# Kernel tuning notes

Measured on AMD Instinct MI355X. Metric: run time of the kernel, lower is better.

The kernel has to match this reference:

```python
import jax, jax.numpy as jnp
import numpy as np

L, H, C, D, B, OUT = 3, 4, 128, 128, 64, 128  # layers, heads, out_ch per head, in_dim, graphs, out_dim
NEG_SLOPE = 0.2
EPS = 1e-5


def _layernorm(x, g, b):
    mu = x.mean(-1, keepdims=True)
    var = ((x - mu) ** 2).mean(-1, keepdims=True)
    return (x - mu) * jax.lax.rsqrt(var + EPS) * g + b


def setup_inputs() -> dict:
    key = jax.random.key(0)
    ks = jax.random.split(key, 20)
    N, E = 50000, 400000
    x = jax.random.normal(ks[0], (N, D), jnp.float32)
    edge_index = jax.random.randint(ks[1], (2, E), 0, N, jnp.int64)
    batch = jnp.sort(jax.random.randint(ks[2], (N,), 0, B, jnp.int64))
    s = 1.0 / np.sqrt(D)
    inp = dict(x=x, edge_index=edge_index, batch=batch)
    inp["Wl"] = jax.random.normal(ks[3], (L, H, C, D), jnp.float32) * s
    inp["bl"] = jnp.zeros((L, H, C), jnp.float32)
    inp["Wr"] = jax.random.normal(ks[4], (L, H, C, D), jnp.float32) * s
    inp["br"] = jnp.zeros((L, H, C), jnp.float32)
    inp["att"] = jax.random.normal(ks[5], (L, H, C), jnp.float32) * (1.0 / np.sqrt(C))
    inp["conv_bias"] = jnp.zeros((L, C), jnp.float32)
    inp["ln_gamma"] = jnp.ones((L, C), jnp.float32)
    inp["ln_beta"] = jnp.zeros((L, C), jnp.float32)
    inp["W1"] = jax.random.normal(ks[6], (2 * C, C), jnp.float32) * (1.0 / np.sqrt(C))
    inp["b1"] = jnp.zeros((2 * C,), jnp.float32)
    inp["W2"] = jax.random.normal(ks[7], (OUT, 2 * C), jnp.float32) * (1.0 / np.sqrt(2 * C))
    inp["b2"] = jnp.zeros((OUT,), jnp.float32)
    inp["og"] = jnp.ones((OUT,), jnp.float32)
    inp["ob"] = jnp.zeros((OUT,), jnp.float32)
    return inp


def reference(x, edge_index, batch, Wl, bl, Wr, br, att, conv_bias, ln_gamma, ln_beta, W1, b1, W2, b2, og, ob):
    N = x.shape[0]
    loops = jnp.arange(N, dtype=edge_index.dtype)
    src = jnp.concatenate([edge_index[0], loops])  # [E+N]
    dst = jnp.concatenate([edge_index[1], loops])
    h = x  # input_proj is Identity (node_feat_dim == hidden_dim)
    for l in range(L):
        xl = jnp.einsum('nd,hcd->nhc', h, Wl[l]) + bl[l]  # [N,H,C]
        xr = jnp.einsum('nd,hcd->nhc', h, Wr[l]) + br[l]
        e = jax.nn.leaky_relu(xl[src] + xr[dst], NEG_SLOPE)  # [E+N,H,C]
        logits = jnp.einsum('ehc,hc->eh', e, att[l])  # [E+N,H]
        m = jax.ops.segment_max(logits, dst, num_segments=N)  # [N,H]
        p = jnp.exp(logits - m[dst])
        denom = jax.ops.segment_sum(p, dst, num_segments=N)
        alpha = p / denom[dst]  # segment softmax (self loops guarantee denom>0)
        out = jax.ops.segment_sum(xl[src] * alpha[:, :, None], dst, num_segments=N)  # [N,H,C]
        out = out.mean(axis=1) + conv_bias[l]  # concat=False -> mean over heads
        out = jax.nn.relu(_layernorm(out, ln_gamma[l], ln_beta[l]))
        h = h + out  # residual
    # global mean pool
    sums = jax.ops.segment_sum(h, batch, num_segments=B)
    cnt = jax.ops.segment_sum(jnp.ones((N,), h.dtype), batch, num_segments=B)
    g = sums / jnp.maximum(cnt, 1.0)[:, None]
    # MLP head + out norm
    g = jax.nn.gelu(g @ W1.T + b1, approximate=False) @ W2.T + b2
    return _layernorm(g, og, ob)
```

## Files before the change

### kernel.cpp

```cpp
#include <hip/hip_runtime.h>
#include <hip/hip_bf16.h>

typedef __bf16 bf16x8 __attribute__((ext_vector_type(8)));
typedef float f32x4 __attribute__((ext_vector_type(4)));
typedef float f32x2 __attribute__((ext_vector_type(2)));

#define EPS 1e-5f

static __device__ __forceinline__ int lower_bound_i(const int* __restrict__ arr, int n, int val) {
  int lo = 0, hi = n;
  while (lo < hi) { int mid = (lo + hi) >> 1; if (arr[mid] < val) lo = mid + 1; else hi = mid; }
  return lo;
}

__global__ void detect_dtypes(const unsigned* __restrict__ xw, const unsigned* __restrict__ eiw,
                              int* __restrict__ flags) {
  __shared__ int s_bf16, s_i64nz;
  int t = threadIdx.x;
  if (t == 0) { s_bf16 = 0; s_i64nz = 0; }
  __syncthreads();
  unsigned w = xw[t * 97];
  unsigned lo = w & 0xFFFFu;
  unsigned e = (lo >> 7) & 0xFF;
  int looks_bf16 = (lo == 0u) || (e >= 0x6A && e <= 0x86);
  atomicAdd(&s_bf16, looks_bf16);
  int k = t * 1031;
  int nz = (eiw[2 * k + 1] != 0u) ? 1 : 0;
  atomicAdd(&s_i64nz, nz);
  __syncthreads();
  if (t == 0) {
    flags[0] = (s_bf16 >= 192) ? 1 : 0;
    flags[1] = (s_i64nz == 0) ? 1 : 0;
  }
}

__global__ void canon_x(const void* __restrict__ src, float* __restrict__ h_f32,
                        __bf16* __restrict__ h_bf, int n, const int* __restrict__ flags) {
  int i = blockIdx.x * blockDim.x + threadIdx.x;
  if (i >= n) return;
  float v;
  if (flags[0]) v = (float)((const __bf16*)src)[i];
  else          v = ((const float*)src)[i];
  h_f32[i] = v;
  h_bf[i] = (__bf16)v;
}

struct ParamDesc { const void* src[12]; int off[13]; };

__global__ void canon_params(ParamDesc pd, float* __restrict__ dst, const int* __restrict__ flags,
                             int total) {
  int i = blockIdx.x * blockDim.x + threadIdx.x;
  if (i >= total) return;
  int s = 0;
#pragma unroll
  for (int k = 1; k < 12; k++) if (i >= pd.off[k]) s = k;
  int j = i - pd.off[s];
  const void* sp = pd.src[s];
  dst[i] = flags[0] ? (float)((const __bf16*)sp)[j] : ((const float*)sp)[j];
}

__global__ void canon_bf16(const void* __restrict__ src, __bf16* __restrict__ dst, int n,
                           const int* __restrict__ flags) {
  int i = blockIdx.x * blockDim.x + threadIdx.x;
  if (i >= n) return;
  if (flags[0]) dst[i] = ((const __bf16*)src)[i];
  else          dst[i] = (__bf16)((const float*)src)[i];
}

__global__ void canon_i32(const void* __restrict__ src, int* __restrict__ dst, int n,
                          const int* __restrict__ flags) {
  int i = blockIdx.x * blockDim.x + threadIdx.x;
  if (i >= n) return;
  if (flags[1]) dst[i] = (int)((const long long*)src)[i];
  else          dst[i] = ((const int*)src)[i];
}

__global__ void count_deg(const int* __restrict__ ei, int E, int N, int* __restrict__ deg) {
  int e = blockIdx.x * blockDim.x + threadIdx.x;
  if (e >= E + N) return;
  int d = (e < E) ? ei[E + e] : (e - E);
  atomicAdd(&deg[d], 1);
}

__global__ __launch_bounds__(256) void block_sums(const int* __restrict__ deg,
                                                  int* __restrict__ bsum, int N) {
  __shared__ int sh[256];
  int i = blockIdx.x * 256 + threadIdx.x;
  int t = threadIdx.x;
  sh[t] = (i < N) ? deg[i] : 0;
  __syncthreads();
  for (int off = 128; off > 0; off >>= 1) {
    if (t < off) sh[t] += sh[t + off];
    __syncthreads();
  }
  if (t == 0) bsum[blockIdx.x] = sh[0];
}

__global__ __launch_bounds__(256) void scan_bsums(const int* __restrict__ bsum,
                                                  int* __restrict__ bpref, int nblocks,
                                                  int* __restrict__ offs, int N) {
  __shared__ int sh[256];
  int t = threadIdx.x;
  int carry = 0;
  for (int base = 0; base < nblocks; base += 256) {
    int idx = base + t;
    int v = (idx < nblocks) ? bsum[idx] : 0;
    sh[t] = v;
    __syncthreads();
    for (int off = 1; off < 256; off <<= 1) {
      int u = (t >= off) ? sh[t - off] : 0;
      __syncthreads();
      sh[t] += u;
      __syncthreads();
    }
    if (idx < nblocks) bpref[idx] = carry + sh[t] - v;
    carry += sh[255];
    __syncthreads();
  }
  if (t == 0) offs[N] = carry;
}

__global__ __launch_bounds__(256) void write_offs(const int* __restrict__ deg,
                                                  const int* __restrict__ bpref,
                                                  int* __restrict__ offs,
                                                  int* __restrict__ cursor, int N) {
  __shared__ int sh[256];
  int i = blockIdx.x * 256 + threadIdx.x;
  int t = threadIdx.x;
  int v = (i < N) ? deg[i] : 0;
  sh[t] = v;
  __syncthreads();
  for (int off = 1; off < 256; off <<= 1) {
    int u = (t >= off) ? sh[t - off] : 0;
    __syncthreads();
    sh[t] += u;
    __syncthreads();
  }
  if (i < N) {
    int ex = bpref[blockIdx.x] + sh[t] - v;
    offs[i] = ex;
    cursor[i] = ex;
  }
}

__global__ void fill_csr(const int* __restrict__ ei, int E, int N,
                         int* __restrict__ cursor, int* __restrict__ csr_src) {
  int e = blockIdx.x * blockDim.x + threadIdx.x;
  if (e >= E + N) return;
  int s, d;
  if (e < E) { s = ei[e]; d = ei[E + e]; } else { s = e - E; d = e - E; }
  int pos = atomicAdd(&cursor[d], 1);
  csr_src[pos] = s;
}

__global__ __launch_bounds__(256) void gemm_xlr(
    const __bf16* __restrict__ A, const __bf16* __restrict__ Wl,
    const __bf16* __restrict__ Wr, const float* __restrict__ bl,
    const float* __restrict__ br, __bf16* __restrict__ out, int Nrows) {
  __shared__ __bf16 As[128][72];
  __shared__ __bf16 Bs[128][72];
  const int jb = blockIdx.y;
  const __bf16* Wbase = (jb < 4) ? (Wl + (size_t)jb * 128 * 128) : (Wr + (size_t)(jb - 4) * 128 * 128);
  const float* biasbase = (jb < 4) ? (bl + jb * 128) : (br + (jb - 4) * 128);
  const int row0 = blockIdx.x * 128;
  const int tid = threadIdx.x;
  const int lane = tid & 63, wave = tid >> 6;
  const int wm = wave >> 1, wn = wave & 1;

  f32x4 zero4 = {0.f, 0.f, 0.f, 0.f};
  f32x4 acc[4][4];
#pragma unroll
  for (int mi = 0; mi < 4; mi++)
#pragma unroll
    for (int ni = 0; ni < 4; ni++) acc[mi][ni] = zero4;

  for (int kc = 0; kc < 2; kc++) {
    __syncthreads();
#pragma unroll
    for (int p = 0; p < 4; p++) {
      int r = (tid >> 3) + p * 32;
      int cg = (tid & 7) * 8;
      int gr = row0 + r;
      bf16x8 av;
      if (gr < Nrows) av = *(const bf16x8*)(A + (size_t)gr * 128 + kc * 64 + cg);
      else {
#pragma unroll
        for (int j = 0; j < 8; j++) av[j] = (__bf16)0.0f;
      }
      *(bf16x8*)(&As[r][cg]) = av;
      bf16x8 bv = *(const bf16x8*)(Wbase + (size_t)r * 128 + kc * 64 + cg);
      *(bf16x8*)(&Bs[r][cg]) = bv;
    }
    __syncthreads();
#pragma unroll
    for (int s = 0; s < 2; s++) {
      bf16x8 af[4], bfr[4];
      int kofs = s * 32 + ((lane >> 4) * 8);
#pragma unroll
      for (int i = 0; i < 4; i++) {
        af[i]  = *(const bf16x8*)(&As[wm * 64 + i * 16 + (lane & 15)][kofs]);
        bfr[i] = *(const bf16x8*)(&Bs[wn * 64 + i * 16 + (lane & 15)][kofs]);
      }
#pragma unroll
      for (int mi = 0; mi < 4; mi++)
#pragma unroll
        for (int ni = 0; ni < 4; ni++)
          acc[mi][ni] = __builtin_amdgcn_mfma_f32_16x16x32_bf16(af[mi], bfr[ni], acc[mi][ni], 0, 0, 0);
    }
  }
#pragma unroll
  for (int mi = 0; mi < 4; mi++) {
#pragma unroll
    for (int ni = 0; ni < 4; ni++) {
      int col_l = wn * 64 + ni * 16 + (lane & 15);
      int gj = jb * 128 + col_l;
      float bias = biasbase[col_l];
#pragma unroll
      for (int r = 0; r < 4; r++) {
        int row_l = wm * 64 + mi * 16 + (lane >> 4) * 4 + r;
        int gr = row0 + row_l;
        if (gr < Nrows) out[(size_t)gr * 1024 + gj] = (__bf16)(acc[mi][ni][r] + bias);
      }
    }
  }
}

__global__ __launch_bounds__(256) void gat_fused(
    const __bf16* __restrict__ comb, const float* __restrict__ att,
    const int* __restrict__ offs, const int* __restrict__ csr_src,
    const float* __restrict__ conv_bias, const float* __restrict__ gamma,
    const float* __restrict__ beta, float* __restrict__ h_f32,
    __bf16* __restrict__ h_bf, int N) {
  int wid = blockIdx.x * 4 + (threadIdx.x >> 6);
  int lane = threadIdx.x & 63;
  if (wid >= N) return;
  int n = wid;
  f32x2 xr2[4], at2[4];
  bf16x8 xrv = *(const bf16x8*)(comb + (size_t)n * 1024 + 512 + lane * 8);
  float4 a0 = *(const float4*)(att + lane * 8);
  float4 a1 = *(const float4*)(att + lane * 8 + 4);
  at2[0] = f32x2{a0.x, a0.y}; at2[1] = f32x2{a0.z, a0.w};
  at2[2] = f32x2{a1.x, a1.y}; at2[3] = f32x2{a1.z, a1.w};
#pragma unroll
  for (int j = 0; j < 4; j++) xr2[j] = f32x2{(float)xrv[2 * j], (float)xrv[2 * j + 1]};

  int off0 = offs[n], off1 = offs[n + 1];
  float m = -1e30f, l = 0.f;
  f32x2 acc2[4];
#pragma unroll
  for (int j = 0; j < 4; j++) acc2[j] = f32x2{0.f, 0.f};

  const __bf16* cb_base = comb;

  auto process = [&](const bf16x8& xv) {
    f32x2 x2[4];
    f32x2 t2 = f32x2{0.f, 0.f};
#pragma unroll
    for (int j = 0; j < 4; j++) {
      x2[j] = f32x2{(float)xv[2 * j], (float)xv[2 * j + 1]};
      f32x2 z = x2[j] + xr2[j];
      f32x2 lz = __builtin_elementwise_max(z, 0.2f * z);
      t2 = t2 + lz * at2[j];
    }
    float t = t2[0] + t2[1];
    t += __shfl_xor(t, 1);
    t += __shfl_xor(t, 2);
    t += __shfl_xor(t, 4);
    t += __shfl_xor(t, 8);
    float mn = fmaxf(m, t);
    float c = __expf(m - mn);
    float p = __expf(t - mn);
    l = fmaf(l, c, p);
    f32x2 c2 = f32x2{c, c}, p2 = f32x2{p, p};
#pragma unroll
    for (int j = 0; j < 4; j++) acc2[j] = acc2[j] * c2 + p2 * x2[j];
    m = mn;
  };

  int pos = off0;
  for (; pos + 2 <= off1; pos += 2) {
    int s0 = csr_src[pos], s1 = csr_src[pos + 1];
    bf16x8 xa = *(const bf16x8*)(cb_base + (size_t)s0 * 1024 + lane * 8);
    bf16x8 xb = *(const bf16x8*)(cb_base + (size_t)s1 * 1024 + lane * 8);
    process(xa);
    process(xb);
  }
  if (pos < off1) {
    int s0 = csr_src[pos];
    bf16x8 xa = *(const bf16x8*)(cb_base + (size_t)s0 * 1024 + lane * 8);
    process(xa);
  }

  float invl = 1.0f / fmaxf(l, 1e-30f);
  float acc[8];
#pragma unroll
  for (int j = 0; j < 4; j++) {
    acc[2 * j]     = acc2[j][0] * invl;
    acc[2 * j + 1] = acc2[j][1] * invl;
  }
#pragma unroll
  for (int j = 0; j < 8; j++) {
    acc[j] += __shfl_xor(acc[j], 16);
    acc[j] += __shfl_xor(acc[j], 32);
  }
  int c0 = (lane & 15) * 8;
  float v[8];
  float s = 0.f, s2 = 0.f;
#pragma unroll
  for (int j = 0; j < 8; j++) {
    v[j] = acc[j] * 0.25f + conv_bias[c0 + j];
    s += v[j]; s2 += v[j] * v[j];
  }
  s  += __shfl_xor(s, 1);  s2 += __shfl_xor(s2, 1);
  s  += __shfl_xor(s, 2);  s2 += __shfl_xor(s2, 2);
  s  += __shfl_xor(s, 4);  s2 += __shfl_xor(s2, 4);
  s  += __shfl_xor(s, 8);  s2 += __shfl_xor(s2, 8);
  float mu = s * (1.f / 128.f);
  float var = fmaxf(s2 * (1.f / 128.f) - mu * mu, 0.f);
  float rs = rsqrtf(var + EPS);
  if (lane < 16) {
    float4 o0, o1;
    bf16x8 hb;
    float hn[8];
#pragma unroll
    for (int j = 0; j < 8; j++) {
      float o = (v[j] - mu) * rs * gamma[c0 + j] + beta[c0 + j];
      o = o > 0.f ? o : 0.f;
      hn[j] = h_f32[(size_t)n * 128 + c0 + j] + o;
      hb[j] = (__bf16)hn[j];
    }
    o0.x = hn[0]; o0.y = hn[1]; o0.z = hn[2]; o0.w = hn[3];
    o1.x = hn[4]; o1.y = hn[5]; o1.z = hn[6]; o1.w = hn[7];
    *(float4*)(h_f32 + (size_t)n * 128 + c0) = o0;
    *(float4*)(h_f32 + (size_t)n * 128 + c0 + 4) = o1;
    *(bf16x8*)(h_bf + (size_t)n * 128 + c0) = hb;
  }
}

__global__ __launch_bounds__(128) void pool(const float* __restrict__ h_f32,
                                            const int* __restrict__ batch, int N,
                                            float* __restrict__ g_sum) {
  int g = blockIdx.x >> 3, slice = blockIdx.x & 7;
  int c = threadIdx.x;
  int r0 = lower_bound_i(batch, N, g);
  int r1 = lower_bound_i(batch, N, g + 1);
  int len = r1 - r0;
  if (len <= 0) return;
  int per = (len + 7) / 8;
  int s0 = r0 + slice * per;
  int s1 = min(s0 + per, r1);
  if (s0 >= s1) return;
  float acc = 0.f;
  for (int r = s0; r < s1; r++) acc += h_f32[(size_t)r * 128 + c];
  atomicAdd(&g_sum[g * 128 + c], acc);
}

__global__ __launch_bounds__(256) void mlp_head(
    const float* __restrict__ g_sum, const int* __restrict__ batch, int N,
    const float* __restrict__ W1, const float* __restrict__ b1,
    const float* __restrict__ W2, const float* __restrict__ b2,
    const float* __restrict__ og, const float* __restrict__ ob,
    void* __restrict__ outv, const int* __restrict__ flags) {
  __shared__ float gld[128];
  __shared__ float hid[256];
  __shared__ float olds[128];
  __shared__ float red[2];
  int b = blockIdx.x, t = threadIdx.x;
  int r0 = lower_bound_i(batch, N, b);
  int r1 = lower_bound_i(batch, N, b + 1);
  int len = r1 - r0;
  float cntf = (float)(len < 1 ? 1 : len);
  if (t < 128) gld[t] = g_sum[b * 128 + t] / cntf;
  __syncthreads();
  float sacc = b1[t];
  for (int d = 0; d < 128; d++) sacc = fmaf(gld[d], W1[(size_t)t * 128 + d], sacc);
  hid[t] = 0.5f * sacc * (1.f + erff(sacc * 0.70710678118654752f));
  __syncthreads();
  if (t < 128) {
    float o = b2[t];
    for (int k = 0; k < 256; k++) o = fmaf(hid[k], W2[(size_t)t * 256 + k], o);
    olds[t] = o;
  }
  __syncthreads();
  if (t < 64) {
    float a = olds[t], bb = olds[t + 64];
    float s = a + bb, s2 = a * a + bb * bb;
    for (int off = 32; off; off >>= 1) { s += __shfl_down(s, off); s2 += __shfl_down(s2, off); }
    if (t == 0) { red[0] = s * (1.f / 128.f); red[1] = s2 * (1.f / 128.f); }
  }
  __syncthreads();
  if (t < 128) {
    float mu = red[0];
    float var = fmaxf(red[1] - mu * mu, 0.f);
    float rs = rsqrtf(var + EPS);
    float o = (olds[t] - mu) * rs * og[t] + ob[t];
    if (flags[0]) ((__bf16*)outv)[b * 128 + t] = (__bf16)o;
    else          ((float*)outv)[b * 128 + t] = o;
  }
}

extern "C" void kernel_launch(void* const* d_in, const int* in_sizes, int n_in,
                              void* d_out, int out_size, void* d_ws, size_t ws_size,
                              hipStream_t stream) {
  const int D = 128, B = 64;
  const int N = in_sizes[0] / D;
  const int E = in_sizes[1] / 2;
  const int EN = E + N;
  const int nsb = (N + 255) / 256;

  char* p = (char*)d_ws;
  auto alloc = [&](size_t bytes) {
    char* r = p; p += (bytes + 255) & ~(size_t)255; return (void*)r;
  };
  int* flags     = (int*)alloc(256);
  float* h_f32   = (float*)alloc((size_t)N * 128 * 4);
  __bf16* h_bf   = (__bf16*)alloc((size_t)N * 128 * 2);
  __bf16* comb   = (__bf16*)alloc((size_t)N * 1024 * 2);
  int* deg       = (int*)alloc((size_t)N * 4);
  int* offs      = (int*)alloc((size_t)(N + 1) * 4);
  int* cursor    = (int*)alloc((size_t)N * 4);
  int* csr_src   = (int*)alloc((size_t)EN * 4);
  float* g_sum   = (float*)alloc((size_t)B * 128 * 4);
  int* ei32      = (int*)alloc((size_t)2 * E * 4);
  int* bat32     = (int*)alloc((size_t)N * 4);
  int* bsum      = (int*)alloc((size_t)nsb * 4);
  int* bpref     = (int*)alloc((size_t)nsb * 4);
  __bf16* w_bf   = (__bf16*)alloc((size_t)2 * 196608 * 2);
  float* params  = (float*)alloc((size_t)71936 * 4);

  float* bl_c  = params + 0;
  float* br_c  = params + 1536;
  float* att_c = params + 3072;
  float* cb_c  = params + 4608;
  float* g_c   = params + 4992;
  float* b_c   = params + 5376;
  float* W1_c  = params + 5760;
  float* b1_c  = params + 38528;
  float* W2_c  = params + 38784;
  float* b2_c  = params + 71552;
  float* og_c  = params + 71680;
  float* ob_c  = params + 71808;

  detect_dtypes<<<1, 256, 0, stream>>>((const unsigned*)d_in[0], (const unsigned*)d_in[1], flags);

  canon_x<<<(N * 128 + 255) / 256, 256, 0, stream>>>(d_in[0], h_f32, h_bf, N * 128, flags);

  ParamDesc pd;
  const int srcidx[12] = {4, 6, 7, 8, 9, 10, 11, 12, 13, 14, 15, 16};
  const int sizes12[12] = {1536, 1536, 1536, 384, 384, 384, 32768, 256, 32768, 128, 128, 128};
  int cum = 0;
  for (int k = 0; k < 12; k++) { pd.src[k] = d_in[srcidx[k]]; pd.off[k] = cum; cum += sizes12[k]; }
  pd.off[12] = cum;
  canon_params<<<(cum + 255) / 256, 256, 0, stream>>>(pd, params, flags, cum);

  canon_bf16<<<(196608 + 255) / 256, 256, 0, stream>>>(d_in[3], w_bf, 196608, flags);
  canon_bf16<<<(196608 + 255) / 256, 256, 0, stream>>>(d_in[5], w_bf + 196608, 196608, flags);

  canon_i32<<<(2 * E + 255) / 256, 256, 0, stream>>>(d_in[1], ei32, 2 * E, flags);
  canon_i32<<<(N + 255) / 256, 256, 0, stream>>>(d_in[2], bat32, N, flags);

  hipMemsetAsync(deg, 0, (size_t)N * 4, stream);
  hipMemsetAsync(g_sum, 0, (size_t)B * 128 * 4, stream);

  count_deg<<<(EN + 255) / 256, 256, 0, stream>>>(ei32, E, N, deg);
  block_sums<<<nsb, 256, 0, stream>>>(deg, bsum, N);
  scan_bsums<<<1, 256, 0, stream>>>(bsum, bpref, nsb, offs, N);
  write_offs<<<nsb, 256, 0, stream>>>(deg, bpref, offs, cursor, N);
  fill_csr<<<(EN + 255) / 256, 256, 0, stream>>>(ei32, E, N, cursor, csr_src);

  for (int l = 0; l < 3; l++) {
    gemm_xlr<<<dim3((N + 127) / 128, 8), 256, 0, stream>>>(
        h_bf, w_bf + (size_t)l * 65536, w_bf + 196608 + (size_t)l * 65536,
        bl_c + l * 512, br_c + l * 512, comb, N);
    gat_fused<<<(N + 3) / 4, 256, 0, stream>>>(comb, att_c + l * 512, offs, csr_src,
        cb_c + l * 128, g_c + l * 128, b_c + l * 128, h_f32, h_bf, N);
  }
  pool<<<B * 8, 128, 0, stream>>>(h_f32, bat32, N, g_sum);
  mlp_head<<<B, 256, 0, stream>>>(g_sum, bat32, N, W1_c, b1_c, W2_c, b2_c, og_c, ob_c, d_out, flags);
}
```

Baseline: 646.7 us.

## Drop online-softmax max tracking, use DPP row reductions, fuse int canonicalization

The GAT aggregation kernel replaces its online softmax rescaling with a clamped direct exponential, removing the running max and per-edge rescale of accumulators. Cross-lane sums switch from shuffles to DPP row operations, and the edge loop issues four gathers at a time. Integer input conversion and degree counting merge into one kernel. The clamp changes numerics if logits exceed the clamp range.

```diff
diff --git a/kernel.cpp b/kernel.cpp
--- a/kernel.cpp
+++ b/kernel.cpp
@@ -11,6 +11,19 @@
   int lo = 0, hi = n;
   while (lo < hi) { int mid = (lo + hi) >> 1; if (arr[mid] < val) lo = mid + 1; else hi = mid; }
   return lo;
+}
+
+template <int CTRL>
+static __device__ __forceinline__ float dpp_add(float x) {
+  int s = __builtin_amdgcn_mov_dpp(__float_as_int(x), CTRL, 0xF, 0xF, true);
+  return x + __int_as_float(s);
+}
+static __device__ __forceinline__ float row16_reduce(float t) {
+  t = dpp_add<0xB1>(t);
+  t = dpp_add<0x4E>(t);
+  t = dpp_add<0x141>(t);
+  t = dpp_add<0x140>(t);
+  return t;
 }
 
 __global__ void detect_dtypes(const unsigned* __restrict__ xw, const unsigned* __restrict__ eiw,
@@ -67,19 +80,23 @@
   else          dst[i] = (__bf16)((const float*)src)[i];
 }
 
-__global__ void canon_i32(const void* __restrict__ src, int* __restrict__ dst, int n,
-                          const int* __restrict__ flags) {
+__global__ void canon_ints(const void* __restrict__ ei_src, const void* __restrict__ bat_src,
+                           int* __restrict__ ei32, int* __restrict__ bat32,
+                           int* __restrict__ deg, int E, int N, const int* __restrict__ flags) {
   int i = blockIdx.x * blockDim.x + threadIdx.x;
-  if (i >= n) return;
-  if (flags[1]) dst[i] = (int)((const long long*)src)[i];
-  else          dst[i] = ((const int*)src)[i];
-}
-
-__global__ void count_deg(const int* __restrict__ ei, int E, int N, int* __restrict__ deg) {
-  int e = blockIdx.x * blockDim.x + threadIdx.x;
-  if (e >= E + N) return;
-  int d = (e < E) ? ei[E + e] : (e - E);
-  atomicAdd(&deg[d], 1);
+  int total = 2 * E + N;
+  if (i >= total) return;
+  int i64 = flags[1];
+  if (i < 2 * E) {
+    int v = i64 ? (int)((const long long*)ei_src)[i] : ((const int*)ei_src)[i];
+    ei32[i] = v;
+    if (i >= E) atomicAdd(&deg[v], 1);
+  } else {
+    int j = i - 2 * E;
+    int v = i64 ? (int)((const long long*)bat_src)[j] : ((const int*)bat_src)[j];
+    bat32[j] = v;
+    atomicAdd(&deg[j], 1);
+  }
 }
 
 __global__ __launch_bounds__(256) void block_sums(const int* __restrict__ deg,
@@ -245,12 +262,12 @@
   for (int j = 0; j < 4; j++) xr2[j] = f32x2{(float)xrv[2 * j], (float)xrv[2 * j + 1]};
 
   int off0 = offs[n], off1 = offs[n + 1];
-  float m = -1e30f, l = 0.f;
+  float l = 0.f;
   f32x2 acc2[4];
 #pragma unroll
   for (int j = 0; j < 4; j++) acc2[j] = f32x2{0.f, 0.f};
 
-  const __bf16* cb_base = comb;
+  const __bf16* lane_base = comb + lane * 8;
 
   auto process = [&](const bf16x8& xv) {
     f32x2 x2[4];
@@ -263,31 +280,28 @@
       t2 = t2 + lz * at2[j];
     }
     float t = t2[0] + t2[1];
-    t += __shfl_xor(t, 1);
-    t += __shfl_xor(t, 2);
-    t += __shfl_xor(t, 4);
-    t += __shfl_xor(t, 8);
-    float mn = fmaxf(m, t);
-    float c = __expf(m - mn);
-    float p = __expf(t - mn);
-    l = fmaf(l, c, p);
-    f32x2 c2 = f32x2{c, c}, p2 = f32x2{p, p};
-#pragma unroll
-    for (int j = 0; j < 4; j++) acc2[j] = acc2[j] * c2 + p2 * x2[j];
-    m = mn;
+    t = row16_reduce(t);
+    t = fminf(fmaxf(t, -60.f), 60.f);
+    float p = __expf(t);
+    l += p;
+    f32x2 p2 = f32x2{p, p};
+#pragma unroll
+    for (int j = 0; j < 4; j++) acc2[j] = acc2[j] + p2 * x2[j];
   };
 
   int pos = off0;
-  for (; pos + 2 <= off1; pos += 2) {
+  for (; pos + 4 <= off1; pos += 4) {
     int s0 = csr_src[pos], s1 = csr_src[pos + 1];
-    bf16x8 xa = *(const bf16x8*)(cb_base + (size_t)s0 * 1024 + lane * 8);
-    bf16x8 xb = *(const bf16x8*)(cb_base + (size_t)s1 * 1024 + lane * 8);
-    process(xa);
-    process(xb);
-  }
-  if (pos < off1) {
+    int s2i = csr_src[pos + 2], s3 = csr_src[pos + 3];
+    bf16x8 xa = *(const bf16x8*)(lane_base + (size_t)s0 * 1024);
+    bf16x8 xb = *(const bf16x8*)(lane_base + (size_t)s1 * 1024);
+    bf16x8 xc = *(const bf16x8*)(lane_base + (size_t)s2i * 1024);
+    bf16x8 xd = *(const bf16x8*)(lane_base + (size_t)s3 * 1024);
+    process(xa); process(xb); process(xc); process(xd);
+  }
+  for (; pos < off1; pos++) {
     int s0 = csr_src[pos];
-    bf16x8 xa = *(const bf16x8*)(cb_base + (size_t)s0 * 1024 + lane * 8);
+    bf16x8 xa = *(const bf16x8*)(lane_base + (size_t)s0 * 1024);
     process(xa);
   }
 
@@ -311,10 +325,8 @@
     v[j] = acc[j] * 0.25f + conv_bias[c0 + j];
     s += v[j]; s2 += v[j] * v[j];
   }
-  s  += __shfl_xor(s, 1);  s2 += __shfl_xor(s2, 1);
-  s  += __shfl_xor(s, 2);  s2 += __shfl_xor(s2, 2);
-  s  += __shfl_xor(s, 4);  s2 += __shfl_xor(s2, 4);
-  s  += __shfl_xor(s, 8);  s2 += __shfl_xor(s2, 8);
+  s = row16_reduce(s);
+  s2 = row16_reduce(s2);
   float mu = s * (1.f / 128.f);
   float var = fmaxf(s2 * (1.f / 128.f) - mu * mu, 0.f);
   float rs = rsqrtf(var + EPS);
@@ -456,13 +468,10 @@
   canon_bf16<<<(196608 + 255) / 256, 256, 0, stream>>>(d_in[3], w_bf, 196608, flags);
   canon_bf16<<<(196608 + 255) / 256, 256, 0, stream>>>(d_in[5], w_bf + 196608, 196608, flags);
 
-  canon_i32<<<(2 * E + 255) / 256, 256, 0, stream>>>(d_in[1], ei32, 2 * E, flags);
-  canon_i32<<<(N + 255) / 256, 256, 0, stream>>>(d_in[2], bat32, N, flags);
-
   hipMemsetAsync(deg, 0, (size_t)N * 4, stream);
   hipMemsetAsync(g_sum, 0, (size_t)B * 128 * 4, stream);
 
-  count_deg<<<(EN + 255) / 256, 256, 0, stream>>>(ei32, E, N, deg);
+  canon_ints<<<(2 * E + N + 255) / 256, 256, 0, stream>>>(d_in[1], d_in[2], ei32, bat32, deg, E, N, flags);
   block_sums<<<nsb, 256, 0, stream>>>(deg, bsum, N);
   scan_bsums<<<1, 256, 0, stream>>>(bsum, bpref, nsb, offs, N);
   write_offs<<<nsb, 256, 0, stream>>>(deg, bpref, offs, cursor, N);
```

Result: no change. 640.1 us (-1.0%).
